# Kernel tuning notes

Hardware: AMD Instinct MI355X
Metric: run time of the kernel (lower is better)

Reference implementation:

```python
import jax, jax.numpy as jnp
import numpy as np

NEG_SLOPE = 0.1

def lrelu(x):
    return jnp.where(x >= 0, x, NEG_SLOPE * x)

def conv1d(x, w, b, stride=2):
    # x: [N, C_in, W], w: [C_out, C_in, K], VALID padding, given stride
    y = jax.lax.conv_general_dilated(x, w, (stride,), 'VALID',
                                     dimension_numbers=('NCH', 'OIH', 'NCH'))
    return y + b[None, :, None]

def setup_inputs() -> dict:
    key = jax.random.key(0)
    ks = jax.random.split(key, 16)
    N_NODES = 50000
    N_EDGES = 4950000
    POS_C, CONV_C, CONV_W = 3, 3, 151
    HID, OUT = 256, 1
    W2 = 37  # width after two stride-2 k=3 convs on 151
    IN_G = POS_C + W2  # 40

    def lin_init(k, fan_out, fan_in):
        s = 1.0 / np.sqrt(fan_in)
        k1, k2 = jax.random.split(k)
        return (jax.random.uniform(k1, (fan_out, fan_in), jnp.float32, -s, s),
                jax.random.uniform(k2, (fan_out,), jnp.float32, -s, s))

    pose = jax.random.normal(ks[0], (N_NODES, POS_C), jnp.float32)
    views = jax.random.normal(ks[1], (N_NODES, CONV_C, CONV_W), jnp.float32)
    edge_index = jax.random.randint(ks[2], (2, N_EDGES), 0, N_NODES, jnp.int64)

    # encoder1: Conv1d(3 -> 9, k=3, s=2); encoder2: Conv1d(9 -> 1, k=3, s=2)
    s1 = 1.0 / np.sqrt(CONV_C * 3)
    w_e1 = jax.random.uniform(ks[3], (CONV_C ** 2, CONV_C, 3), jnp.float32, -s1, s1)
    b_e1 = jax.random.uniform(ks[4], (CONV_C ** 2,), jnp.float32, -s1, s1)
    s2 = 1.0 / np.sqrt(CONV_C ** 2 * 3)
    w_e2 = jax.random.uniform(ks[5], (1, CONV_C ** 2, 3), jnp.float32, -s2, s2)
    b_e2 = jax.random.uniform(ks[6], (1,), jnp.float32, -s2, s2)

    # GraphConv: lin_rel (with bias) on aggregated neighbors, lin_root (no bias) on self
    w_rel, b_rel = lin_init(ks[7], HID, IN_G)
    w_root, _ = lin_init(ks[8], HID, IN_G)

    w_l1, b_l1 = lin_init(ks[9], HID, HID)
    w_l2, b_l2 = lin_init(ks[10], HID, HID)
    w_l3, b_l3 = lin_init(ks[11], HID, HID)
    w_pred, b_pred = lin_init(ks[12], OUT, HID)

    return dict(pose=pose, views=views, edge_index=edge_index,
                w_e1=w_e1, b_e1=b_e1, w_e2=w_e2, b_e2=b_e2,
                w_rel=w_rel, b_rel=b_rel, w_root=w_root,
                w_l1=w_l1, b_l1=b_l1, w_l2=w_l2, b_l2=b_l2,
                w_l3=w_l3, b_l3=b_l3, w_pred=w_pred, b_pred=b_pred)

def reference(pose, views, edge_index, w_e1, b_e1, w_e2, b_e2,
              w_rel, b_rel, w_root,
              w_l1, b_l1, w_l2, b_l2, w_l3, b_l3, w_pred, b_pred):
    n_nodes = pose.shape[0]
    # view encoder
    v = lrelu(conv1d(views, w_e1, b_e1))          # [N, 9, 75]
    v = lrelu(conv1d(v, w_e2, b_e2))              # [N, 1, 37]
    x = jnp.concatenate([pose, v[:, 0, :]], axis=1)  # [N, 40]
    # GraphConv (aggr='add'): out = lin_rel(sum_{j->i} x_j) + lin_root(x_i)
    src, dst = edge_index[0], edge_index[1]
    agg = jax.ops.segment_sum(x[src], dst, num_segments=n_nodes)  # [N, 40]
    h = lrelu(agg @ w_rel.T + b_rel + x @ w_root.T)               # [N, 256]
    # MLP stack (dropout is identity in eval mode)
    h = lrelu(h @ w_l1.T + b_l1)
    h = lrelu(h @ w_l2.T + b_l2)
    h = lrelu(h @ w_l3.T + b_l3)
    return h @ w_pred.T + b_pred  # [N, 1]
```

## Files before the change

### kernel.cpp

```cpp
#include <hip/hip_runtime.h>
#include <hip/hip_fp16.h>

#define NEG_SLOPE 0.1f
__device__ __forceinline__ float lrelu(float v) { return fmaxf(v, NEG_SLOPE * v); }

constexpr int CAP = 8704;
constexpr int EPB = 8192;

typedef __attribute__((ext_vector_type(8))) short short8;
typedef __attribute__((ext_vector_type(4))) float f32x4;
typedef __attribute__((ext_vector_type(2))) float f32x2;
typedef __attribute__((ext_vector_type(4))) int i32x4;

__device__ __forceinline__ unsigned short f2bf(float f) {
    union { float f; unsigned u; } v; v.f = f;
    const unsigned r = v.u + 0x7FFF + ((v.u >> 16) & 1);
    return (unsigned short)(r >> 16);
}
__device__ __forceinline__ float bf2f(unsigned short h) {
    union { unsigned u; float f; } v; v.u = ((unsigned)h) << 16;
    return v.f;
}

__global__ __launch_bounds__(256) void encoder_kernel(
        const float* __restrict__ pose,
        const float* __restrict__ views,
        const float* __restrict__ w1, const float* __restrict__ b1,
        const float* __restrict__ w2, const float* __restrict__ b2,
        const float* __restrict__ w_l1, const float* __restrict__ w_l2,
        const float* __restrict__ w_l3, const float* __restrict__ w_rel,
        const float* __restrict__ w_root,
        unsigned short* __restrict__ Wb1, unsigned short* __restrict__ Wb2,
        unsigned short* __restrict__ Wb3, unsigned short* __restrict__ Wg,
        int* __restrict__ gcur,
        unsigned short* __restrict__ xHi, unsigned short* __restrict__ xLo,
        __half* __restrict__ xh, int N)
{
    __shared__ float s_w1[81];
    __shared__ float s_b1[9];
    __shared__ float s_w2[27];
    __shared__ float s_b2[1];
    __shared__ float s_c1[4][9][80];

    const int t = threadIdx.x;

    if (blockIdx.x < 256) {
        const int i = blockIdx.x * 256 + t;
        Wb1[i] = f2bf(w_l1[i]);
        Wb2[i] = f2bf(w_l2[i]);
        Wb3[i] = f2bf(w_l3[i]);
        if (i < 40960) {
            const int m = i / 160, c = i % 160;
            const int k = c % 80;
            const float v = (k < 40) ? w_rel[m * 40 + k] : w_root[m * 40 + (k - 40)];
            Wg[i] = f2bf(v);
        }
        if (i < 1024) gcur[i] = 0;
        if (i < 40) xh[(size_t)N * 40 + i] = __float2half(0.f);
    }

    if (t < 81) s_w1[t] = w1[t];
    if (t >= 96 && t < 105) s_b1[t - 96] = b1[t - 96];
    if (t >= 128 && t < 155) s_w2[t - 128] = w2[t - 128];
    if (t == 240) s_b2[0] = b2[0];
    __syncthreads();

    const int nb = blockIdx.x * 4;

    #pragma unroll
    for (int pass = 0; pass < 2; pass++) {
        const int task = pass * 256 + t;
        if (task < 300) {
            const int ln = task / 75;
            const int p  = task % 75;
            const int n  = min(nb + ln, N - 1);
            const float* __restrict__ vin = views + (size_t)n * 453 + 2 * p;
            float e[3], o[3], e1[3];
            #pragma unroll
            for (int ic = 0; ic < 3; ic++) {
                const float* ci = vin + ic * 151;
                e[ic] = ci[0]; o[ic] = ci[1]; e1[ic] = ci[2];
            }
            const int didx = (p & 1) * 40 + (p >> 1);
            #pragma unroll
            for (int oc = 0; oc < 9; oc++) {
                float v = s_b1[oc];
                #pragma unroll
                for (int ic = 0; ic < 3; ic++)
                    v += s_w1[oc * 9 + ic * 3 + 0] * e[ic]
                       + s_w1[oc * 9 + ic * 3 + 1] * o[ic]
                       + s_w1[oc * 9 + ic * 3 + 2] * e1[ic];
                s_c1[ln][oc][didx] = lrelu(v);
            }
        }
    }
    __syncthreads();

    if (t < 160) {
        const int ln = t / 40, f = t % 40;
        const int n  = min(nb + ln, N - 1);
        float outv;
        if (f < 3) {
            outv = pose[(size_t)n * 3 + f];
        } else {
            const int ow = f - 3;
            float v = s_b2[0];
            #pragma unroll
            for (int ic = 0; ic < 9; ic++)
                v += s_w2[ic * 3 + 0] * s_c1[ln][ic][ow]
                   + s_w2[ic * 3 + 1] * s_c1[ln][ic][40 + ow]
                   + s_w2[ic * 3 + 2] * s_c1[ln][ic][ow + 1];
            outv = lrelu(v);
        }
        const unsigned short hi = f2bf(outv);
        const unsigned short lo = f2bf(outv - bf2f(hi));
        xHi[(size_t)n * 40 + f] = hi;
        xLo[(size_t)n * 40 + f] = lo;
        xh[(size_t)n * 40 + f] = __float2half(outv);
    }
}

__global__ __launch_bounds__(512) void bin_kernel(
        const int* __restrict__ ei, int* __restrict__ gcur,
        int* __restrict__ pairs, int E, int NB)
{
    __shared__ int s_hist[1024];
    __shared__ int s_loff[1024];
    __shared__ int s_base[1024];
    __shared__ int s_wave8[8];
    __shared__ int s_pk[EPB];
    __shared__ unsigned short s_bkt[EPB];
    const int t = threadIdx.x;
    const int lane = t & 63, wid = t >> 6;
    const int e0 = blockIdx.x * EPB + t * 16;
    const int tot = min(E - (int)blockIdx.x * EPB, EPB);

    for (int i = t; i < 1024; i += 512) s_hist[i] = 0;
    __syncthreads();

    int pk[16], mt[16];
    auto proc = [&](int j, int sv, int dv) {
        const int b = dv >> 6;
        const int r = atomicAdd(&s_hist[b], 1);
        pk[j] = sv * 80 | ((dv & 63) << 22);
        mt[j] = b | (r << 10);
    };

    if (e0 + 16 <= E) {
        #pragma unroll
        for (int q = 0; q < 4; q++) {
            const int4 sv = *(const int4*)(ei + e0 + 4 * q);
            const int4 dv = *(const int4*)(ei + E + e0 + 4 * q);
            proc(4 * q + 0, sv.x, dv.x);
            proc(4 * q + 1, sv.y, dv.y);
            proc(4 * q + 2, sv.z, dv.z);
            proc(4 * q + 3, sv.w, dv.w);
        }
    } else {
        #pragma unroll
        for (int j = 0; j < 16; j++) {
            mt[j] = -1;
            const int e = e0 + j;
            if (e < E) proc(j, ei[e], ei[E + e]);
        }
    }
    __syncthreads();

    int carry = 0;
    #pragma unroll
    for (int base = 0; base < 1024; base += 512) {
        const int i = base + t;
        const int v = s_hist[i];
        int sc = v;
        #pragma unroll
        for (int d = 1; d < 64; d <<= 1) {
            const int u = __shfl_up(sc, d);
            if (lane >= d) sc += u;
        }
        if (lane == 63) s_wave8[wid] = sc;
        __syncthreads();
        if (wid == 0) {
            int wv = (lane < 8) ? s_wave8[lane] : 0;
            #pragma unroll
            for (int d = 1; d < 8; d <<= 1) {
                const int u = __shfl_up(wv, d);
                if (lane >= d) wv += u;
            }
            if (lane < 8) s_wave8[lane] = wv;
        }
        __syncthreads();
        const int waveoff = (wid > 0) ? s_wave8[wid - 1] : 0;
        s_loff[i] = carry + waveoff + sc - v;
        const int chunk_tot = s_wave8[7];
        __syncthreads();
        carry += chunk_tot;
    }

    for (int i = t; i < NB; i += 512) {
        const int c = s_hist[i];
        if (c > 0) s_base[i] = atomicAdd(&gcur[i], c);
    }
    __syncthreads();

    #pragma unroll
    for (int j = 0; j < 16; j++) {
        if (mt[j] >= 0) {
            const int b = mt[j] & 1023;
            const int pos = s_loff[b] + (mt[j] >> 10);
            s_pk[pos] = pk[j];
            s_bkt[pos] = (unsigned short)b;
        }
    }
    __syncthreads();

    for (int i = t; i < tot; i += 512) {
        const int b = s_bkt[i];
        const int p = s_base[b] + (i - s_loff[b]);
        if (p < CAP) pairs[b * CAP + p] = s_pk[i];
    }
}

__global__ __launch_bounds__(512) void sort_gather_kernel(
        const int* __restrict__ gcur,
        const int* __restrict__ pairs,
        const __half* __restrict__ xh,
        unsigned short* __restrict__ aggHi,
        unsigned short* __restrict__ aggLo, int N)
{
    __shared__ int s_sorted[CAP];
    __shared__ int s_cnt[64], s_off[64];
    const int b = blockIdx.x;
    const int t = threadIdx.x;
    const int cnt = min(gcur[b], CAP);
    const int* __restrict__ pr = pairs + (size_t)b * CAP;

    if (t < 64) s_cnt[t] = 0;

    int pk[17];
    {
        const i32x4* __restrict__ pr4 = (const i32x4*)pr;
        #pragma unroll
        for (int j = 0; j < 4; j++) {
            const int m = t + j * 512;
            const i32x4 v = __builtin_nontemporal_load(pr4 + m);
            const int e0 = m * 4;
            pk[4 * j + 0] = (e0 + 0 < cnt) ? v.x : -1;
            pk[4 * j + 1] = (e0 + 1 < cnt) ? v.y : -1;
            pk[4 * j + 2] = (e0 + 2 < cnt) ? v.z : -1;
            pk[4 * j + 3] = (e0 + 3 < cnt) ? v.w : -1;
        }
        const int m16 = 8192 + t;
        pk[16] = (m16 < cnt) ? __builtin_nontemporal_load(pr + m16) : -1;
    }
    __syncthreads();

    int rk[17];
    #pragma unroll
    for (int j = 0; j < 17; j++)
        if (pk[j] >= 0) rk[j] = atomicAdd(&s_cnt[pk[j] >> 22], 1);
    __syncthreads();

    if (t < 64) {
        const int c = s_cnt[t];
        const int p = ((c + 23) / 24) * 24;
        int sc = p;
        #pragma unroll
        for (int d = 1; d < 64; d <<= 1) {
            const int u = __shfl_up(sc, d);
            if (t >= d) sc += u;
        }
        s_off[t] = sc - p;
    }
    __syncthreads();

    if (t < 64) {
        const int e0 = s_off[t] + s_cnt[t];
        const int e1 = s_off[t] + ((s_cnt[t] + 23) / 24) * 24;
        for (int i = e0; i < e1 && i < CAP; i++) s_sorted[i] = N * 80;
    }
    #pragma unroll
    for (int j = 0; j < 17; j++) {
        if (pk[j] >= 0) {
            const int pos = s_off[pk[j] >> 22] + rk[j];
            if (pos < CAP) s_sorted[pos] = pk[j] & 0x3FFFFF;
        }
    }
    __syncthreads();

    const int wave = t >> 6, lane = t & 63;
    const int slot = min(lane / 5, 11);
    const int f8 = lane % 5;
    const char* __restrict__ xb = (const char*)xh + f8 * 16;

    #pragma unroll 1
    for (int i = 0; i < 8; i++) {
        const int ln = wave * 8 + i;
        const int n = b * 64 + ln;
        if (n >= N) break;
        const int c = s_cnt[ln];
        const int cntp = ((c + 23) / 24) * 24;
        const int* __restrict__ srt = s_sorted + s_off[ln] + slot;

        f32x2 a0 = {0.f, 0.f}, a1 = {0.f, 0.f}, a2 = {0.f, 0.f}, a3 = {0.f, 0.f};

        union { unsigned v; __half2 h; } cv;
        auto cv2 = [&](unsigned u) -> f32x2 {
            cv.v = u;
            const float2 ff = __half22float2(cv.h);
            f32x2 r; r.x = ff.x; r.y = ff.y; return r;
        };
        auto acc8 = [&](uint4 u) {
            a0 += cv2(u.x); a1 += cv2(u.y); a2 += cv2(u.z); a3 += cv2(u.w);
        };

        int e = 0;
        #pragma unroll 1
        for (; e + 48 <= cntp; e += 48) {
            const int o0 = srt[e];
            const int o1 = srt[e + 12];
            const int o2 = srt[e + 24];
            const int o3 = srt[e + 36];
            const uint4 u0 = *(const uint4*)(xb + o0);
            const uint4 u1 = *(const uint4*)(xb + o1);
            const uint4 u2 = *(const uint4*)(xb + o2);
            const uint4 u3 = *(const uint4*)(xb + o3);
            acc8(u0); acc8(u1); acc8(u2); acc8(u3);
        }
        if (e < cntp) {
            const int o0 = srt[e];
            const int o1 = srt[e + 12];
            const uint4 u0 = *(const uint4*)(xb + o0);
            const uint4 u1 = *(const uint4*)(xb + o1);
            acc8(u0); acc8(u1);
        }

        #pragma unroll
        for (int st = 0; st < 2; st++) {
            const int d = st ? 15 : 30;
            a0.x += __shfl(a0.x, lane + d); a0.y += __shfl(a0.y, lane + d);
            a1.x += __shfl(a1.x, lane + d); a1.y += __shfl(a1.y, lane + d);
            a2.x += __shfl(a2.x, lane + d); a2.y += __shfl(a2.y, lane + d);
            a3.x += __shfl(a3.x, lane + d); a3.y += __shfl(a3.y, lane + d);
        }
        a0.x += __shfl(a0.x, lane + 5) + __shfl(a0.x, lane + 10);
        a0.y += __shfl(a0.y, lane + 5) + __shfl(a0.y, lane + 10);
        a1.x += __shfl(a1.x, lane + 5) + __shfl(a1.x, lane + 10);
        a1.y += __shfl(a1.y, lane + 5) + __shfl(a1.y, lane + 10);
        a2.x += __shfl(a2.x, lane + 5) + __shfl(a2.x, lane + 10);
        a2.y += __shfl(a2.y, lane + 5) + __shfl(a2.y, lane + 10);
        a3.x += __shfl(a3.x, lane + 5) + __shfl(a3.x, lane + 10);
        a3.y += __shfl(a3.y, lane + 5) + __shfl(a3.y, lane + 10);

        if (lane < 5) {
            const float av[8] = {a0.x, a0.y, a1.x, a1.y, a2.x, a2.y, a3.x, a3.y};
            unsigned short h[8], l[8];
            #pragma unroll
            for (int j = 0; j < 8; j++) {
                h[j] = f2bf(av[j]);
                l[j] = f2bf(av[j] - bf2f(h[j]));
            }
            uint4 H, L;
            H.x = h[0] | ((unsigned)h[1] << 16); H.y = h[2] | ((unsigned)h[3] << 16);
            H.z = h[4] | ((unsigned)h[5] << 16); H.w = h[6] | ((unsigned)h[7] << 16);
            L.x = l[0] | ((unsigned)l[1] << 16); L.y = l[2] | ((unsigned)l[3] << 16);
            L.z = l[4] | ((unsigned)l[5] << 16); L.w = l[6] | ((unsigned)l[7] << 16);
            *(uint4*)(aggHi + (size_t)n * 40 + lane * 8) = H;
            *(uint4*)(aggLo + (size_t)n * 40 + lane * 8) = L;
        }
    }
}

__device__ __forceinline__ int aswz(int row, int col) {
    return row * 256 + (col ^ ((row & 7) << 3));
}

__device__ __forceinline__ void gload16(const void* g, void* l) {
    __builtin_amdgcn_global_load_lds(
        (const __attribute__((address_space(1))) unsigned int*)g,
        (__attribute__((address_space(3))) unsigned int*)l,
        16, 0, 0);
}

__device__ __forceinline__ void stage_panel(const unsigned short* __restrict__ W,
                                            int wstride, int k0,
                                            unsigned short* buf, int wave, int lane)
{
    const int rbase = wave * 64 + (lane >> 2);
    const int cu = (lane & 3) * 8;
    #pragma unroll
    for (int j = 0; j < 4; j++) {
        const int row = rbase + j * 16;
        gload16(W + (size_t)row * wstride + k0 + cu,
                buf + (wave * 4 + j) * 512);
    }
}

__device__ __forceinline__ void gemm_layer(const unsigned short* __restrict__ aT,
                                           const unsigned short* __restrict__ W,
                                           int wstride, int K,
                                           unsigned short* __restrict__ sW0,
                                           unsigned short* __restrict__ sW1,
                                           int wave, int lane, int l16, int q,
                                           f32x4 acc[4][4])
{
    const int NP = K >> 5;
    stage_panel(W, wstride, 0, sW0, wave, lane);
    stage_panel(W, wstride, 32, sW1, wave, lane);
    const int wrow = (wave * 64 + l16) * 32 + q * 8;

    for (int p = 0; p < NP; p++) {
        unsigned short* wb = (p & 1) ? sW1 : sW0;
        if (p + 1 < NP) asm volatile("s_waitcnt vmcnt(4)" ::: "memory");
        else            asm volatile("s_waitcnt vmcnt(0)" ::: "memory");
        short8 af[4], wf[4];
        #pragma unroll
        for (int nt = 0; nt < 4; nt++)
            af[nt] = *(const short8*)(aT + aswz(nt * 16 + l16, p * 32 + q * 8));
        #pragma unroll
        for (int mt = 0; mt < 4; mt++)
            wf[mt] = *(const short8*)(wb + wrow + mt * 16 * 32);
        if (p + 2 < NP) {
            asm volatile("s_waitcnt lgkmcnt(0)" ::: "memory");
            __builtin_amdgcn_sched_barrier(0);
            stage_panel(W, wstride, (p + 2) * 32, wb, wave, lane);
        }
        #pragma unroll
        for (int nt = 0; nt < 4; nt++)
            #pragma unroll
            for (int mt = 0; mt < 4; mt++)
                acc[nt][mt] = __builtin_amdgcn_mfma_f32_16x16x32_bf16(af[nt], wf[mt], acc[nt][mt], 0, 0, 0);
    }
}

__device__ __forceinline__ void epi_to_lds(f32x4 acc[4][4], const float* __restrict__ b,
                                           unsigned short* __restrict__ aT,
                                           int wave, int l16, int q)
{
    float bias[4];
    #pragma unroll
    for (int mt = 0; mt < 4; mt++) bias[mt] = b[wave * 64 + mt * 16 + l16];
    #pragma unroll
    for (int nt = 0; nt < 4; nt++)
        #pragma unroll
        for (int r = 0; r < 4; r++)
            #pragma unroll
            for (int mt = 0; mt < 4; mt++) {
                const int row = nt * 16 + q * 4 + r;
                const int col = wave * 64 + mt * 16 + l16;
                aT[aswz(row, col)] = f2bf(lrelu(acc[nt][mt][r] + bias[mt]));
            }
}

__global__ __launch_bounds__(256) void fused_gemm_kernel(
                                  const unsigned short* __restrict__ aggHi,
                                  const unsigned short* __restrict__ aggLo,
                                  const unsigned short* __restrict__ xHi,
                                  const unsigned short* __restrict__ xLo,
                                  const unsigned short* __restrict__ Wg,
                                  const float* __restrict__ b_rel,
                                  const unsigned short* __restrict__ Wb1,
                                  const float* __restrict__ b_l1,
                                  const unsigned short* __restrict__ Wb2,
                                  const float* __restrict__ b_l2,
                                  const unsigned short* __restrict__ Wb3,
                                  const float* __restrict__ b_l3,
                                  const float* __restrict__ w_pred,
                                  const float* __restrict__ b_pred,
                                  float* __restrict__ out, int N)
{
    __shared__ __align__(16) unsigned short aT[64 * 256];
    __shared__ __align__(16) unsigned short sW[2][256 * 32];
    const int t = threadIdx.x;
    const int n0 = blockIdx.x * 64;
    const int wave = t >> 6, lane = t & 63, q = lane >> 4, l16 = lane & 15;

    for (int u = t; u < 640; u += 256) {
        const int row = u / 10, c = (u % 10) * 4;
        const int srow = min(n0 + row, N - 1);
        const size_t off = (size_t)srow * 40 + c;
        *(ushort4*)(aT + aswz(row, c))       = *(const ushort4*)(aggHi + off);
        *(ushort4*)(aT + aswz(row, 40 + c))  = *(const ushort4*)(xHi + off);
        *(ushort4*)(aT + aswz(row, 80 + c))  = *(const ushort4*)(aggLo + off);
        *(ushort4*)(aT + aswz(row, 120 + c)) = *(const ushort4*)(xLo + off);
    }
    __syncthreads();

    {
        f32x4 acc[4][4] = {};
        gemm_layer(aT, Wg, 160, 160, sW[0], sW[1], wave, lane, l16, q, acc);
        __syncthreads();
        epi_to_lds(acc, b_rel, aT, wave, l16, q);
        __syncthreads();
    }
    {
        f32x4 acc[4][4] = {};
        gemm_layer(aT, Wb1, 256, 256, sW[0], sW[1], wave, lane, l16, q, acc);
        __syncthreads();
        epi_to_lds(acc, b_l1, aT, wave, l16, q);
        __syncthreads();
    }
    {
        f32x4 acc[4][4] = {};
        gemm_layer(aT, Wb2, 256, 256, sW[0], sW[1], wave, lane, l16, q, acc);
        __syncthreads();
        epi_to_lds(acc, b_l2, aT, wave, l16, q);
        __syncthreads();
    }
    {
        f32x4 acc[4][4] = {};
        gemm_layer(aT, Wb3, 256, 256, sW[0], sW[1], wave, lane, l16, q, acc);

        float bias[4], wp[4];
        #pragma unroll
        for (int mt = 0; mt < 4; mt++) {
            const int col = wave * 64 + mt * 16 + l16;
            bias[mt] = b_l3[col];
            wp[mt] = w_pred[col];
        }
        float* spw = (float*)(sW[0] + (wave * 4) * 512);
        #pragma unroll
        for (int nt = 0; nt < 4; nt++)
            #pragma unroll
            for (int r = 0; r < 4; r++) {
                float p = 0.f;
                #pragma unroll
                for (int mt = 0; mt < 4; mt++)
                    p += lrelu(acc[nt][mt][r] + bias[mt]) * wp[mt];
                p += __shfl_xor(p, 1);
                p += __shfl_xor(p, 2);
                p += __shfl_xor(p, 4);
                p += __shfl_xor(p, 8);
                if (l16 == 0) spw[nt * 16 + q * 4 + r] = p;
            }
        __syncthreads();

        if (t < 64) {
            const int row = n0 + t;
            if (row < N) {
                float s = b_pred[0];
                #pragma unroll
                for (int w = 0; w < 4; w++)
                    s += ((const float*)(sW[0] + (w * 4) * 512))[t];
                out[row] = s;
            }
        }
    }
}

extern "C" void kernel_launch(void* const* d_in, const int* in_sizes, int n_in,
                              void* d_out, int out_size, void* d_ws, size_t ws_size,
                              hipStream_t stream)
{
    const float* pose   = (const float*)d_in[0];
    const float* views  = (const float*)d_in[1];
    const int*   ei     = (const int*)d_in[2];
    const float* w_e1   = (const float*)d_in[3];
    const float* b_e1   = (const float*)d_in[4];
    const float* w_e2   = (const float*)d_in[5];
    const float* b_e2   = (const float*)d_in[6];
    const float* w_rel  = (const float*)d_in[7];
    const float* b_rel  = (const float*)d_in[8];
    const float* w_root = (const float*)d_in[9];
    const float* w_l1   = (const float*)d_in[10];
    const float* b_l1   = (const float*)d_in[11];
    const float* w_l2   = (const float*)d_in[12];
    const float* b_l2   = (const float*)d_in[13];
    const float* w_l3   = (const float*)d_in[14];
    const float* b_l3   = (const float*)d_in[15];
    const float* w_pred = (const float*)d_in[16];
    const float* b_pred = (const float*)d_in[17];
    float* out = (float*)d_out;

    const int N = in_sizes[0] / 3;
    const int E = in_sizes[2] / 2;
    const int NB = (N + 63) >> 6;
    const int NBLK = (N + 63) / 64;

    unsigned short* xHi = (unsigned short*)d_ws;
    unsigned short* xLo = xHi + (size_t)N * 40;
    unsigned short* aggHi = xLo + (size_t)N * 40;
    unsigned short* aggLo = aggHi + (size_t)N * 40;
    __half* xh = (__half*)(aggLo + (size_t)N * 40);
    int* pairs = (int*)(xh + (size_t)(N + 1) * 40 + 24);
    int* gcur  = pairs + (size_t)NB * CAP;
    unsigned short* Wb1 = (unsigned short*)(gcur + 1024);
    unsigned short* Wb2 = Wb1 + 256 * 256;
    unsigned short* Wb3 = Wb2 + 256 * 256;
    unsigned short* Wg  = Wb3 + 256 * 256;

    encoder_kernel<<<(N + 3) / 4, 256, 0, stream>>>(
        pose, views, w_e1, b_e1, w_e2, b_e2,
        w_l1, w_l2, w_l3, w_rel, w_root,
        Wb1, Wb2, Wb3, Wg, gcur, xHi, xLo, xh, N);

    bin_kernel<<<(E + EPB - 1) / EPB, 512, 0, stream>>>(ei, gcur, pairs, E, NB);

    sort_gather_kernel<<<NB, 512, 0, stream>>>(gcur, pairs, xh, aggHi, aggLo, N);

    fused_gemm_kernel<<<NBLK, 256, 0, stream>>>(
        aggHi, aggLo, xHi, xLo, Wg, b_rel,
        Wb1, b_l1, Wb2, b_l2, Wb3, b_l3,
        w_pred, b_pred, out, N);
}
```

Measured before the change: 326.9 us.

## Fuse neighbor sort-gather with MLP GEMM stack into one kernel

```diff
diff --git a/kernel.cpp b/kernel.cpp
--- a/kernel.cpp
+++ b/kernel.cpp
@@ -142,7 +142,7 @@
     auto proc = [&](int j, int sv, int dv) {
         const int b = dv >> 6;
         const int r = atomicAdd(&s_hist[b], 1);
-        pk[j] = sv * 80 | ((dv & 63) << 22);
+        pk[j] = sv | ((dv & 63) << 22);
         mt[j] = b | (r << 10);
     };
 
@@ -220,17 +220,115 @@
     }
 }
 
-__global__ __launch_bounds__(512) void sort_gather_kernel(
+__device__ __forceinline__ int aswz(int row, int col) {
+    return row * 256 + (col ^ ((row & 7) << 3));
+}
+
+__device__ __forceinline__ void gload16(const void* g, void* l) {
+    __builtin_amdgcn_global_load_lds(
+        (const __attribute__((address_space(1))) unsigned int*)g,
+        (__attribute__((address_space(3))) unsigned int*)l,
+        16, 0, 0);
+}
+
+__device__ __forceinline__ void stage_panel(const unsigned short* __restrict__ W,
+                                            int wstride, int k0,
+                                            unsigned short* buf, int wave, int lane)
+{
+    const int rbase = wave * 32 + (lane >> 2);
+    const int cu = (lane & 3) * 8;
+    #pragma unroll
+    for (int j = 0; j < 2; j++) {
+        const int row = rbase + j * 16;
+        gload16(W + (size_t)row * wstride + k0 + cu,
+                buf + (wave * 2 + j) * 512);
+    }
+}
+
+__device__ __forceinline__ void gemm_layer(const unsigned short* __restrict__ aT,
+                                           const unsigned short* __restrict__ W,
+                                           int wstride, int K,
+                                           unsigned short* __restrict__ sWb,
+                                           int wave, int lane, int l16, int q,
+                                           f32x4 acc[4][2])
+{
+    const int NP = K >> 5;
+    stage_panel(W, wstride, 0,  sWb,        wave, lane);
+    stage_panel(W, wstride, 32, sWb + 8192, wave, lane);
+    const int wro = (wave * 2) * 512 + l16 * 32 + q * 8;
+
+    for (int p = 0; p < NP; p++) {
+        unsigned short* wb = sWb + (p & 1) * 8192;
+        if (p + 1 < NP) asm volatile("s_waitcnt vmcnt(2)" ::: "memory");
+        else            asm volatile("s_waitcnt vmcnt(0)" ::: "memory");
+        short8 af[4], wf[2];
+        #pragma unroll
+        for (int nt = 0; nt < 4; nt++)
+            af[nt] = *(const short8*)(aT + aswz(nt * 16 + l16, p * 32 + q * 8));
+        #pragma unroll
+        for (int mt = 0; mt < 2; mt++)
+            wf[mt] = *(const short8*)(wb + wro + mt * 512);
+        if (p + 2 < NP) {
+            asm volatile("s_waitcnt lgkmcnt(0)" ::: "memory");
+            __builtin_amdgcn_sched_barrier(0);
+            stage_panel(W, wstride, (p + 2) * 32, wb, wave, lane);
+        }
+        #pragma unroll
+        for (int nt = 0; nt < 4; nt++)
+            #pragma unroll
+            for (int mt = 0; mt < 2; mt++)
+                acc[nt][mt] = __builtin_amdgcn_mfma_f32_16x16x32_bf16(af[nt], wf[mt], acc[nt][mt], 0, 0, 0);
+    }
+}
+
+__device__ __forceinline__ void epi_to_lds(f32x4 acc[4][2], const float* __restrict__ b,
+                                           unsigned short* __restrict__ aT,
+                                           int wave, int l16, int q)
+{
+    float bias[2];
+    #pragma unroll
+    for (int mt = 0; mt < 2; mt++) bias[mt] = b[wave * 32 + mt * 16 + l16];
+    #pragma unroll
+    for (int nt = 0; nt < 4; nt++)
+        #pragma unroll
+        for (int r = 0; r < 4; r++)
+            #pragma unroll
+            for (int mt = 0; mt < 2; mt++) {
+                const int row = nt * 16 + q * 4 + r;
+                const int col = wave * 32 + mt * 16 + l16;
+                aT[aswz(row, col)] = f2bf(lrelu(acc[nt][mt][r] + bias[mt]));
+            }
+}
+
+__global__ __launch_bounds__(512) void sg_gemm_kernel(
         const int* __restrict__ gcur,
         const int* __restrict__ pairs,
         const __half* __restrict__ xh,
-        unsigned short* __restrict__ aggHi,
-        unsigned short* __restrict__ aggLo, int N)
-{
-    __shared__ int s_sorted[CAP];
-    __shared__ int s_cnt[64], s_off[64];
+        const unsigned short* __restrict__ xHi,
+        const unsigned short* __restrict__ xLo,
+        const unsigned short* __restrict__ Wg,
+        const float* __restrict__ b_rel,
+        const unsigned short* __restrict__ Wb1,
+        const float* __restrict__ b_l1,
+        const unsigned short* __restrict__ Wb2,
+        const float* __restrict__ b_l2,
+        const unsigned short* __restrict__ Wb3,
+        const float* __restrict__ b_l3,
+        const float* __restrict__ w_pred,
+        const float* __restrict__ b_pred,
+        float* __restrict__ out, int N)
+{
+    __shared__ __align__(16) unsigned short aT[64 * 256];
+    __shared__ __align__(16) char uni[32768];
+    unsigned short* s_sorted = (unsigned short*)uni;
+    int* s_cnt = (int*)(uni + 17408);
+    int* s_off = (int*)(uni + 17664);
+    unsigned short* sWb = (unsigned short*)uni;
+
     const int b = blockIdx.x;
     const int t = threadIdx.x;
+    const int n0 = b * 64;
+    const int wave = t >> 6, lane = t & 63, q = lane >> 4, l16 = lane & 15;
     const int cnt = min(gcur[b], CAP);
     const int* __restrict__ pr = pairs + (size_t)b * CAP;
 
@@ -252,6 +350,13 @@
         const int m16 = 8192 + t;
         pk[16] = (m16 < cnt) ? __builtin_nontemporal_load(pr + m16) : -1;
     }
+    for (int u = t; u < 640; u += 512) {
+        const int row = u / 10, c = (u % 10) * 4;
+        const int srow = min(n0 + row, N - 1);
+        const size_t off = (size_t)srow * 40 + c;
+        *(ushort4*)(aT + aswz(row, 40 + c))  = *(const ushort4*)(xHi + off);
+        *(ushort4*)(aT + aswz(row, 120 + c)) = *(const ushort4*)(xLo + off);
+    }
     __syncthreads();
 
     int rk[17];
@@ -276,255 +381,140 @@
     if (t < 64) {
         const int e0 = s_off[t] + s_cnt[t];
         const int e1 = s_off[t] + ((s_cnt[t] + 23) / 24) * 24;
-        for (int i = e0; i < e1 && i < CAP; i++) s_sorted[i] = N * 80;
+        for (int i = e0; i < e1 && i < CAP; i++) s_sorted[i] = (unsigned short)N;
     }
     #pragma unroll
     for (int j = 0; j < 17; j++) {
         if (pk[j] >= 0) {
             const int pos = s_off[pk[j] >> 22] + rk[j];
-            if (pos < CAP) s_sorted[pos] = pk[j] & 0x3FFFFF;
-        }
-    }
-    __syncthreads();
-
-    const int wave = t >> 6, lane = t & 63;
-    const int slot = min(lane / 5, 11);
-    const int f8 = lane % 5;
-    const char* __restrict__ xb = (const char*)xh + f8 * 16;
-
-    #pragma unroll 1
-    for (int i = 0; i < 8; i++) {
-        const int ln = wave * 8 + i;
-        const int n = b * 64 + ln;
-        if (n >= N) break;
-        const int c = s_cnt[ln];
-        const int cntp = ((c + 23) / 24) * 24;
-        const int* __restrict__ srt = s_sorted + s_off[ln] + slot;
-
-        f32x2 a0 = {0.f, 0.f}, a1 = {0.f, 0.f}, a2 = {0.f, 0.f}, a3 = {0.f, 0.f};
-
-        union { unsigned v; __half2 h; } cv;
-        auto cv2 = [&](unsigned u) -> f32x2 {
-            cv.v = u;
-            const float2 ff = __half22float2(cv.h);
-            f32x2 r; r.x = ff.x; r.y = ff.y; return r;
-        };
-        auto acc8 = [&](uint4 u) {
-            a0 += cv2(u.x); a1 += cv2(u.y); a2 += cv2(u.z); a3 += cv2(u.w);
-        };
-
-        int e = 0;
+            if (pos < CAP) s_sorted[pos] = (unsigned short)(pk[j] & 0xFFFF);
+        }
+    }
+    __syncthreads();
+
+    {
+        const int slot = min(lane / 5, 11);
+        const int f8 = lane % 5;
+        const char* __restrict__ xb = (const char*)xh + f8 * 16;
+
         #pragma unroll 1
-        for (; e + 48 <= cntp; e += 48) {
-            const int o0 = srt[e];
-            const int o1 = srt[e + 12];
-            const int o2 = srt[e + 24];
-            const int o3 = srt[e + 36];
-            const uint4 u0 = *(const uint4*)(xb + o0);
-            const uint4 u1 = *(const uint4*)(xb + o1);
-            const uint4 u2 = *(const uint4*)(xb + o2);
-            const uint4 u3 = *(const uint4*)(xb + o3);
-            acc8(u0); acc8(u1); acc8(u2); acc8(u3);
-        }
-        if (e < cntp) {
-            const int o0 = srt[e];
-            const int o1 = srt[e + 12];
-            const uint4 u0 = *(const uint4*)(xb + o0);
-            const uint4 u1 = *(const uint4*)(xb + o1);
-            acc8(u0); acc8(u1);
-        }
-
-        #pragma unroll
-        for (int st = 0; st < 2; st++) {
-            const int d = st ? 15 : 30;
-            a0.x += __shfl(a0.x, lane + d); a0.y += __shfl(a0.y, lane + d);
-            a1.x += __shfl(a1.x, lane + d); a1.y += __shfl(a1.y, lane + d);
-            a2.x += __shfl(a2.x, lane + d); a2.y += __shfl(a2.y, lane + d);
-            a3.x += __shfl(a3.x, lane + d); a3.y += __shfl(a3.y, lane + d);
-        }
-        a0.x += __shfl(a0.x, lane + 5) + __shfl(a0.x, lane + 10);
-        a0.y += __shfl(a0.y, lane + 5) + __shfl(a0.y, lane + 10);
-        a1.x += __shfl(a1.x, lane + 5) + __shfl(a1.x, lane + 10);
-        a1.y += __shfl(a1.y, lane + 5) + __shfl(a1.y, lane + 10);
-        a2.x += __shfl(a2.x, lane + 5) + __shfl(a2.x, lane + 10);
-        a2.y += __shfl(a2.y, lane + 5) + __shfl(a2.y, lane + 10);
-        a3.x += __shfl(a3.x, lane + 5) + __shfl(a3.x, lane + 10);
-        a3.y += __shfl(a3.y, lane + 5) + __shfl(a3.y, lane + 10);
-
-        if (lane < 5) {
-            const float av[8] = {a0.x, a0.y, a1.x, a1.y, a2.x, a2.y, a3.x, a3.y};
-            unsigned short h[8], l[8];
-            #pragma unroll
-            for (int j = 0; j < 8; j++) {
-                h[j] = f2bf(av[j]);
-                l[j] = f2bf(av[j] - bf2f(h[j]));
-            }
-            uint4 H, L;
-            H.x = h[0] | ((unsigned)h[1] << 16); H.y = h[2] | ((unsigned)h[3] << 16);
-            H.z = h[4] | ((unsigned)h[5] << 16); H.w = h[6] | ((unsigned)h[7] << 16);
-            L.x = l[0] | ((unsigned)l[1] << 16); L.y = l[2] | ((unsigned)l[3] << 16);
-            L.z = l[4] | ((unsigned)l[5] << 16); L.w = l[6] | ((unsigned)l[7] << 16);
-            *(uint4*)(aggHi + (size_t)n * 40 + lane * 8) = H;
-            *(uint4*)(aggLo + (size_t)n * 40 + lane * 8) = L;
-        }
-    }
-}
-
-__device__ __forceinline__ int aswz(int row, int col) {
-    return row * 256 + (col ^ ((row & 7) << 3));
-}
-
-__device__ __forceinline__ void gload16(const void* g, void* l) {
-    __builtin_amdgcn_global_load_lds(
-        (const __attribute__((address_space(1))) unsigned int*)g,
-        (__attribute__((address_space(3))) unsigned int*)l,
-        16, 0, 0);
-}
-
-__device__ __forceinline__ void stage_panel(const unsigned short* __restrict__ W,
-                                            int wstride, int k0,
-                                            unsigned short* buf, int wave, int lane)
-{
-    const int rbase = wave * 64 + (lane >> 2);
-    const int cu = (lane & 3) * 8;
-    #pragma unroll
-    for (int j = 0; j < 4; j++) {
-        const int row = rbase + j * 16;
-        gload16(W + (size_t)row * wstride + k0 + cu,
-                buf + (wave * 4 + j) * 512);
-    }
-}
-
-__device__ __forceinline__ void gemm_layer(const unsigned short* __restrict__ aT,
-                                           const unsigned short* __restrict__ W,
-                                           int wstride, int K,
-                                           unsigned short* __restrict__ sW0,
-                                           unsigned short* __restrict__ sW1,
-                                           int wave, int lane, int l16, int q,
-                                           f32x4 acc[4][4])
-{
-    const int NP = K >> 5;
-    stage_panel(W, wstride, 0, sW0, wave, lane);
-    stage_panel(W, wstride, 32, sW1, wave, lane);
-    const int wrow = (wave * 64 + l16) * 32 + q * 8;
-
-    for (int p = 0; p < NP; p++) {
-        unsigned short* wb = (p & 1) ? sW1 : sW0;
-        if (p + 1 < NP) asm volatile("s_waitcnt vmcnt(4)" ::: "memory");
-        else            asm volatile("s_waitcnt vmcnt(0)" ::: "memory");
-        short8 af[4], wf[4];
-        #pragma unroll
-        for (int nt = 0; nt < 4; nt++)
-            af[nt] = *(const short8*)(aT + aswz(nt * 16 + l16, p * 32 + q * 8));
-        #pragma unroll
-        for (int mt = 0; mt < 4; mt++)
-            wf[mt] = *(const short8*)(wb + wrow + mt * 16 * 32);
-        if (p + 2 < NP) {
-            asm volatile("s_waitcnt lgkmcnt(0)" ::: "memory");
-            __builtin_amdgcn_sched_barrier(0);
-            stage_panel(W, wstride, (p + 2) * 32, wb, wave, lane);
-        }
-        #pragma unroll
-        for (int nt = 0; nt < 4; nt++)
-            #pragma unroll
-            for (int mt = 0; mt < 4; mt++)
-                acc[nt][mt] = __builtin_amdgcn_mfma_f32_16x16x32_bf16(af[nt], wf[mt], acc[nt][mt], 0, 0, 0);
-    }
-}
-
-__device__ __forceinline__ void epi_to_lds(f32x4 acc[4][4], const float* __restrict__ b,
-                                           unsigned short* __restrict__ aT,
-                                           int wave, int l16, int q)
-{
-    float bias[4];
-    #pragma unroll
-    for (int mt = 0; mt < 4; mt++) bias[mt] = b[wave * 64 + mt * 16 + l16];
-    #pragma unroll
-    for (int nt = 0; nt < 4; nt++)
-        #pragma unroll
-        for (int r = 0; r < 4; r++)
-            #pragma unroll
-            for (int mt = 0; mt < 4; mt++) {
-                const int row = nt * 16 + q * 4 + r;
-                const int col = wave * 64 + mt * 16 + l16;
-                aT[aswz(row, col)] = f2bf(lrelu(acc[nt][mt][r] + bias[mt]));
-            }
-}
-
-__global__ __launch_bounds__(256) void fused_gemm_kernel(
-                                  const unsigned short* __restrict__ aggHi,
-                                  const unsigned short* __restrict__ aggLo,
-                                  const unsigned short* __restrict__ xHi,
-                                  const unsigned short* __restrict__ xLo,
-                                  const unsigned short* __restrict__ Wg,
-                                  const float* __restrict__ b_rel,
-                                  const unsigned short* __restrict__ Wb1,
-                                  const float* __restrict__ b_l1,
-                                  const unsigned short* __restrict__ Wb2,
-                                  const float* __restrict__ b_l2,
-                                  const unsigned short* __restrict__ Wb3,
-                                  const float* __restrict__ b_l3,
-                                  const float* __restrict__ w_pred,
-                                  const float* __restrict__ b_pred,
-                                  float* __restrict__ out, int N)
-{
-    __shared__ __align__(16) unsigned short aT[64 * 256];
-    __shared__ __align__(16) unsigned short sW[2][256 * 32];
-    const int t = threadIdx.x;
-    const int n0 = blockIdx.x * 64;
-    const int wave = t >> 6, lane = t & 63, q = lane >> 4, l16 = lane & 15;
-
-    for (int u = t; u < 640; u += 256) {
-        const int row = u / 10, c = (u % 10) * 4;
-        const int srow = min(n0 + row, N - 1);
-        const size_t off = (size_t)srow * 40 + c;
-        *(ushort4*)(aT + aswz(row, c))       = *(const ushort4*)(aggHi + off);
-        *(ushort4*)(aT + aswz(row, 40 + c))  = *(const ushort4*)(xHi + off);
-        *(ushort4*)(aT + aswz(row, 80 + c))  = *(const ushort4*)(aggLo + off);
-        *(ushort4*)(aT + aswz(row, 120 + c)) = *(const ushort4*)(xLo + off);
+        for (int i = 0; i < 8; i++) {
+            const int ln = wave * 8 + i;
+            const int n = n0 + ln;
+            if (n >= N) break;
+            const int c = s_cnt[ln];
+            const int cntp = ((c + 23) / 24) * 24;
+            const unsigned short* __restrict__ srt = s_sorted + s_off[ln] + slot;
+
+            f32x2 a0 = {0.f, 0.f}, a1 = {0.f, 0.f}, a2 = {0.f, 0.f}, a3 = {0.f, 0.f};
+            union { unsigned v; __half2 h; } cv;
+            auto cv2 = [&](unsigned u) -> f32x2 {
+                cv.v = u;
+                const float2 ff = __half22float2(cv.h);
+                f32x2 r; r.x = ff.x; r.y = ff.y; return r;
+            };
+            auto acc8 = [&](uint4 u) {
+                a0 += cv2(u.x); a1 += cv2(u.y); a2 += cv2(u.z); a3 += cv2(u.w);
+            };
+
+            int e = 0;
+            #pragma unroll 1
+            for (; e + 48 <= cntp; e += 48) {
+                const int o0 = srt[e] * 80;
+                const int o1 = srt[e + 12] * 80;
+                const int o2 = srt[e + 24] * 80;
+                const int o3 = srt[e + 36] * 80;
+                const uint4 u0 = *(const uint4*)(xb + o0);
+                const uint4 u1 = *(const uint4*)(xb + o1);
+                const uint4 u2 = *(const uint4*)(xb + o2);
+                const uint4 u3 = *(const uint4*)(xb + o3);
+                acc8(u0); acc8(u1); acc8(u2); acc8(u3);
+            }
+            if (e < cntp) {
+                const int o0 = srt[e] * 80;
+                const int o1 = srt[e + 12] * 80;
+                const uint4 u0 = *(const uint4*)(xb + o0);
+                const uint4 u1 = *(const uint4*)(xb + o1);
+                acc8(u0); acc8(u1);
+            }
+
+            #pragma unroll
+            for (int st = 0; st < 2; st++) {
+                const int d = st ? 15 : 30;
+                a0.x += __shfl(a0.x, lane + d); a0.y += __shfl(a0.y, lane + d);
+                a1.x += __shfl(a1.x, lane + d); a1.y += __shfl(a1.y, lane + d);
+                a2.x += __shfl(a2.x, lane + d); a2.y += __shfl(a2.y, lane + d);
+                a3.x += __shfl(a3.x, lane + d); a3.y += __shfl(a3.y, lane + d);
+            }
+            a0.x += __shfl(a0.x, lane + 5) + __shfl(a0.x, lane + 10);
+            a0.y += __shfl(a0.y, lane + 5) + __shfl(a0.y, lane + 10);
+            a1.x += __shfl(a1.x, lane + 5) + __shfl(a1.x, lane + 10);
+            a1.y += __shfl(a1.y, lane + 5) + __shfl(a1.y, lane + 10);
+            a2.x += __shfl(a2.x, lane + 5) + __shfl(a2.x, lane + 10);
+            a2.y += __shfl(a2.y, lane + 5) + __shfl(a2.y, lane + 10);
+            a3.x += __shfl(a3.x, lane + 5) + __shfl(a3.x, lane + 10);
+            a3.y += __shfl(a3.y, lane + 5) + __shfl(a3.y, lane + 10);
+
+            if (lane < 5) {
+                const float av[8] = {a0.x, a0.y, a1.x, a1.y, a2.x, a2.y, a3.x, a3.y};
+                unsigned short h[8], l[8];
+                #pragma unroll
+                for (int j = 0; j < 8; j++) {
+                    h[j] = f2bf(av[j]);
+                    l[j] = f2bf(av[j] - bf2f(h[j]));
+                }
+                uint4 H, L;
+                H.x = h[0] | ((unsigned)h[1] << 16); H.y = h[2] | ((unsigned)h[3] << 16);
+                H.z = h[4] | ((unsigned)h[5] << 16); H.w = h[6] | ((unsigned)h[7] << 16);
+                L.x = l[0] | ((unsigned)l[1] << 16); L.y = l[2] | ((unsigned)l[3] << 16);
+                L.z = l[4] | ((unsigned)l[5] << 16); L.w = l[6] | ((unsigned)l[7] << 16);
+                *(uint4*)(aT + aswz(ln, lane * 8))      = H;
+                *(uint4*)(aT + aswz(ln, 80 + lane * 8)) = L;
+            }
+        }
     }
     __syncthreads();
 
     {
-        f32x4 acc[4][4] = {};
-        gemm_layer(aT, Wg, 160, 160, sW[0], sW[1], wave, lane, l16, q, acc);
+        f32x4 acc[4][2] = {};
+        gemm_layer(aT, Wg, 160, 160, sWb, wave, lane, l16, q, acc);
         __syncthreads();
         epi_to_lds(acc, b_rel, aT, wave, l16, q);
         __syncthreads();
     }
     {
-        f32x4 acc[4][4] = {};
-        gemm_layer(aT, Wb1, 256, 256, sW[0], sW[1], wave, lane, l16, q, acc);
+        f32x4 acc[4][2] = {};
+        gemm_layer(aT, Wb1, 256, 256, sWb, wave, lane, l16, q, acc);
         __syncthreads();
         epi_to_lds(acc, b_l1, aT, wave, l16, q);
         __syncthreads();
     }
     {
-        f32x4 acc[4][4] = {};
-        gemm_layer(aT, Wb2, 256, 256, sW[0], sW[1], wave, lane, l16, q, acc);
+        f32x4 acc[4][2] = {};
+        gemm_layer(aT, Wb2, 256, 256, sWb, wave, lane, l16, q, acc);
         __syncthreads();
         epi_to_lds(acc, b_l2, aT, wave, l16, q);
         __syncthreads();
     }
     {
-        f32x4 acc[4][4] = {};
-        gemm_layer(aT, Wb3, 256, 256, sW[0], sW[1], wave, lane, l16, q, acc);
-
-        float bias[4], wp[4];
-        #pragma unroll
-        for (int mt = 0; mt < 4; mt++) {
-            const int col = wave * 64 + mt * 16 + l16;
+        f32x4 acc[4][2] = {};
+        gemm_layer(aT, Wb3, 256, 256, sWb, wave, lane, l16, q, acc);
+
+        float bias[2], wp[2];
+        #pragma unroll
+        for (int mt = 0; mt < 2; mt++) {
+            const int col = wave * 32 + mt * 16 + l16;
             bias[mt] = b_l3[col];
             wp[mt] = w_pred[col];
         }
-        float* spw = (float*)(sW[0] + (wave * 4) * 512);
+        float* spw = (float*)(uni + wave * 2048);
         #pragma unroll
         for (int nt = 0; nt < 4; nt++)
             #pragma unroll
             for (int r = 0; r < 4; r++) {
                 float p = 0.f;
                 #pragma unroll
-                for (int mt = 0; mt < 4; mt++)
+                for (int mt = 0; mt < 2; mt++)
                     p += lrelu(acc[nt][mt][r] + bias[mt]) * wp[mt];
                 p += __shfl_xor(p, 1);
                 p += __shfl_xor(p, 2);
@@ -539,8 +529,8 @@
             if (row < N) {
                 float s = b_pred[0];
                 #pragma unroll
-                for (int w = 0; w < 4; w++)
-                    s += ((const float*)(sW[0] + (w * 4) * 512))[t];
+                for (int w = 0; w < 8; w++)
+                    s += ((const float*)(uni + w * 2048))[t];
                 out[row] = s;
             }
         }
@@ -574,13 +564,10 @@
     const int N = in_sizes[0] / 3;
     const int E = in_sizes[2] / 2;
     const int NB = (N + 63) >> 6;
-    const int NBLK = (N + 63) / 64;
 
     unsigned short* xHi = (unsigned short*)d_ws;
     unsigned short* xLo = xHi + (size_t)N * 40;
-    unsigned short* aggHi = xLo + (size_t)N * 40;
-    unsigned short* aggLo = aggHi + (size_t)N * 40;
-    __half* xh = (__half*)(aggLo + (size_t)N * 40);
+    __half* xh = (__half*)(xLo + (size_t)N * 40);
     int* pairs = (int*)(xh + (size_t)(N + 1) * 40 + 24);
     int* gcur  = pairs + (size_t)NB * CAP;
     unsigned short* Wb1 = (unsigned short*)(gcur + 1024);
@@ -595,10 +582,8 @@
 
     bin_kernel<<<(E + EPB - 1) / EPB, 512, 0, stream>>>(ei, gcur, pairs, E, NB);
 
-    sort_gather_kernel<<<NB, 512, 0, stream>>>(gcur, pairs, xh, aggHi, aggLo, N);
-
-    fused_gemm_kernel<<<NBLK, 256, 0, stream>>>(
-        aggHi, aggLo, xHi, xLo, Wg, b_rel,
+    sg_gemm_kernel<<<NB, 512, 0, stream>>>(
+        gcur, pairs, xh, xHi, xLo, Wg, b_rel,
         Wb1, b_l1, Wb2, b_l2, Wb3, b_l3,
         w_pred, b_pred, out, N);
 }
```

After: 325.1 us. About the same (-0.6%).
